# Performance work log

Measured on AMD Instinct MI355X. Metric: run time of the kernel, lower is better.

## Reference

```python
import jax, jax.numpy as jnp
import numpy as np

N_NODES = 100000
N_EDGES = 1250000
D_FEAT = 64


def setup_inputs() -> dict:
    key = jax.random.key(0)
    kx, ke = jax.random.split(key)
    x = jax.random.normal(kx, (N_NODES, D_FEAT), dtype=jnp.float32)
    edge_index = jax.random.randint(ke, (2, N_EDGES), 0, N_NODES, dtype=jnp.int64)
    return {"x": x, "edge_index": edge_index}


def reference(x, edge_index):
    # adj[src, dst] = 1; x_neighbors = adj.T @ x  ->
    # x_neighbors[i] = sum_{edges (s, d) with d == i} x[s]
    src, dst = edge_index[0], edge_index[1]
    msgs = x[src]  # [n_edges, d_feat] gather
    x_neighbors = jax.ops.segment_sum(msgs, dst, num_segments=x.shape[0])
    return x_neighbors
```

## Files before the change

kernel.cpp:

```cpp
#include <hip/hip_runtime.h>
#include <hip/hip_bf16.h>

#define N_NODES 100000
#define N_EDGES 1250000
#define D_FEAT  64
#define SB_NODES 512
#define SB_SHIFT 9
#define NSB     196
#define CAP_SB  7040
#define OVF_CAP 8192
#define EPB_I4  1024
#define N_I4    (N_EDGES / 4)
#define NBLK_BUILD ((N_I4 + EPB_I4 - 1) / EPB_I4)
#define RT      512

__global__ __launch_bounds__(256) void to_bf16(
    const float* __restrict__ x, ushort* __restrict__ xh)
{
    int t = blockIdx.x * 256 + threadIdx.x;
    const float4* x4 = (const float4*)x;
    float4 a = x4[2 * t];
    float4 b = x4[2 * t + 1];
    float f[8] = {a.x, a.y, a.z, a.w, b.x, b.y, b.z, b.w};
    uint h[8];
#pragma unroll
    for (int i = 0; i < 8; ++i) {
        uint u = __float_as_uint(f[i]);
        u += 0x7FFFu + ((u >> 16) & 1u);
        h[i] = u >> 16;
    }
    uint4 o;
    o.x = h[0] | (h[1] << 16);
    o.y = h[2] | (h[3] << 16);
    o.z = h[4] | (h[5] << 16);
    o.w = h[6] | (h[7] << 16);
    ((uint4*)xh)[t] = o;
}

__global__ __launch_bounds__(256) void build_sb(
    const int* __restrict__ src, const int* __restrict__ dst,
    uint* __restrict__ fill, uint* __restrict__ pairs,
    uint* __restrict__ ovfCnt, int2* __restrict__ ovf)
{
    __shared__ uint cnt[NSB];
    __shared__ uint base[NSB];
    const int t = threadIdx.x;
    for (int i = t; i < NSB; i += 256) cnt[i] = 0;
    __syncthreads();

    uint   pw[16];
    ushort pb[16];
    ushort pr[16];
    bool   vk[4];
    const int i40 = blockIdx.x * EPB_I4;
#pragma unroll
    for (int k = 0; k < 4; ++k) {
        int i4 = i40 + t + k * 256;
        vk[k] = (i4 < N_I4);
        if (vk[k]) {
            int4 d4 = ((const int4*)dst)[i4];
            int4 s4 = ((const int4*)src)[i4];
            int dd[4] = {d4.x, d4.y, d4.z, d4.w};
            int ss[4] = {s4.x, s4.y, s4.z, s4.w};
#pragma unroll
            for (int j = 0; j < 4; ++j) {
                uint b = ((uint)dd[j]) >> SB_SHIFT;
                uint r = atomicAdd(&cnt[b], 1u);
                pw[k * 4 + j] = ((((uint)dd[j]) & (SB_NODES - 1u)) << 17) | (uint)ss[j];
                pb[k * 4 + j] = (ushort)b;
                pr[k * 4 + j] = (ushort)r;
            }
        }
    }
    __syncthreads();

    for (int i = t; i < NSB; i += 256) {
        uint c = cnt[i];
        base[i] = c ? atomicAdd(&fill[i], c) : 0u;
    }
    __syncthreads();

#pragma unroll
    for (int j = 0; j < 16; ++j) {
        if (vk[j >> 2]) {
            uint b = pb[j];
            uint g = base[b] + pr[j];
            if (g < CAP_SB) {
                pairs[(size_t)b * CAP_SB + g] = pw[j];
            } else {
                uint o = atomicAdd(ovfCnt, 1u);
                if (o < OVF_CAP)
                    ovf[o] = make_int2((int)(pw[j] & 0x1FFFFu),
                                       (int)((b << SB_SHIFT) | (pw[j] >> 17)));
            }
        }
    }
}

__global__ __launch_bounds__(RT) void repart(
    uint* __restrict__ pairs, const uint* __restrict__ fill,
    uint* __restrict__ offs)
{
    __shared__ uint pw[CAP_SB];
    __shared__ int  cnt[SB_NODES];
    __shared__ int  scn[SB_NODES];
    __shared__ int  pos[SB_NODES];

    const int t  = threadIdx.x;
    const int sb = blockIdx.x;
    const int n  = min((int)fill[sb], CAP_SB);
    const size_t base = (size_t)sb * CAP_SB;

    cnt[t] = 0;
    __syncthreads();
    for (int i = t; i < n; i += RT) {
        uint w = pairs[base + i];
        pw[i] = w;
        atomicAdd(&cnt[w >> 17], 1);
    }
    __syncthreads();

    scn[t] = cnt[t];
    __syncthreads();
    for (int off = 1; off < SB_NODES; off <<= 1) {
        int v = (t >= off) ? scn[t - off] : 0;
        __syncthreads();
        scn[t] += v;
        __syncthreads();
    }
    {
        int e = scn[t] - cnt[t];
        pos[t] = e;
        offs[sb * SB_NODES + t] = (uint)e | ((uint)cnt[t] << 16);
    }
    __syncthreads();

    for (int i = t; i < n; i += RT) {
        uint w = pw[i];
        int r = atomicAdd(&pos[w >> 17], 1);
        pairs[base + r] = w & 0x1FFFFu;
    }
}

__global__ __launch_bounds__(256) void gather_csr(
    const ushort* __restrict__ xh, const uint* __restrict__ pairs,
    const uint* __restrict__ offs, float* __restrict__ out)
{
    const int t    = threadIdx.x;
    const int wid  = t >> 6;
    const int lane = t & 63;
    const int sub  = lane >> 3;
    const int l8   = lane & 7;
    const uint4* __restrict__ xrow = (const uint4*)xh;

    for (int nl = wid; nl < 64; nl += 4) {
        const int node = blockIdx.x * 64 + nl;
        if (node >= N_NODES) break;
        const uint v    = offs[node];
        const int start = (node >> SB_SHIFT) * CAP_SB + (int)(v & 0xFFFFu);
        const int deg   = (int)(v >> 16);

        float f[8];
#pragma unroll
        for (int j = 0; j < 8; ++j) f[j] = 0.f;

        int i = sub;
        for (; i + 8 < deg; i += 16) {
            uint s0 = pairs[start + i];
            uint s1 = pairs[start + i + 8];
            uint4 v0 = xrow[(size_t)s0 * 8 + l8];
            uint4 v1 = xrow[(size_t)s1 * 8 + l8];
            f[0] += __uint_as_float((v0.x & 0xFFFFu) << 16);
            f[1] += __uint_as_float(v0.x & 0xFFFF0000u);
            f[2] += __uint_as_float((v0.y & 0xFFFFu) << 16);
            f[3] += __uint_as_float(v0.y & 0xFFFF0000u);
            f[4] += __uint_as_float((v0.z & 0xFFFFu) << 16);
            f[5] += __uint_as_float(v0.z & 0xFFFF0000u);
            f[6] += __uint_as_float((v0.w & 0xFFFFu) << 16);
            f[7] += __uint_as_float(v0.w & 0xFFFF0000u);
            f[0] += __uint_as_float((v1.x & 0xFFFFu) << 16);
            f[1] += __uint_as_float(v1.x & 0xFFFF0000u);
            f[2] += __uint_as_float((v1.y & 0xFFFFu) << 16);
            f[3] += __uint_as_float(v1.y & 0xFFFF0000u);
            f[4] += __uint_as_float((v1.z & 0xFFFFu) << 16);
            f[5] += __uint_as_float(v1.z & 0xFFFF0000u);
            f[6] += __uint_as_float((v1.w & 0xFFFFu) << 16);
            f[7] += __uint_as_float(v1.w & 0xFFFF0000u);
        }
        if (i < deg) {
            uint s0 = pairs[start + i];
            uint4 v0 = xrow[(size_t)s0 * 8 + l8];
            f[0] += __uint_as_float((v0.x & 0xFFFFu) << 16);
            f[1] += __uint_as_float(v0.x & 0xFFFF0000u);
            f[2] += __uint_as_float((v0.y & 0xFFFFu) << 16);
            f[3] += __uint_as_float(v0.y & 0xFFFF0000u);
            f[4] += __uint_as_float((v0.z & 0xFFFFu) << 16);
            f[5] += __uint_as_float(v0.z & 0xFFFF0000u);
            f[6] += __uint_as_float((v0.w & 0xFFFFu) << 16);
            f[7] += __uint_as_float(v0.w & 0xFFFF0000u);
        }

#pragma unroll
        for (int j = 0; j < 8; ++j) {
            f[j] += __shfl_xor(f[j], 8, 64);
            f[j] += __shfl_xor(f[j], 16, 64);
            f[j] += __shfl_xor(f[j], 32, 64);
        }

        if (lane < 8) {
            float4* out4 = (float4*)out;
            out4[(size_t)node * 16 + l8 * 2]     = make_float4(f[0], f[1], f[2], f[3]);
            out4[(size_t)node * 16 + l8 * 2 + 1] = make_float4(f[4], f[5], f[6], f[7]);
        }
    }
}

__global__ __launch_bounds__(256) void ovf_fixup(
    const float* __restrict__ x, const int2* __restrict__ ovf,
    const uint* __restrict__ ovfCnt, float* __restrict__ out)
{
    const int n = min((int)*ovfCnt, OVF_CAP);
    const int wave = (blockIdx.x * blockDim.x + threadIdx.x) >> 6;
    const int lane = threadIdx.x & 63;
    const int nwaves = (gridDim.x * blockDim.x) >> 6;
    for (int e = wave; e < n; e += nwaves) {
        int2 p = ovf[e];
        atomicAdd(&out[(size_t)p.y * D_FEAT + lane], x[(size_t)p.x * D_FEAT + lane]);
    }
}

extern "C" void kernel_launch(void* const* d_in, const int* in_sizes, int n_in,
                              void* d_out, int out_size, void* d_ws, size_t ws_size,
                              hipStream_t stream) {
    const float* x = (const float*)d_in[0];
    const int* edge_index = (const int*)d_in[1];
    const int* src = edge_index;
    const int* dst = edge_index + N_EDGES;
    float* out = (float*)d_out;

    ushort* xh     = (ushort*)d_ws;
    uint*   pairs  = (uint*)(xh + (size_t)N_NODES * D_FEAT);
    uint*   offs   = pairs + (size_t)NSB * CAP_SB;
    uint*   fill   = offs + NSB * SB_NODES;
    uint*   ovfCnt = fill + NSB;
    int2*   ovf    = (int2*)(fill + NSB + 2);

    hipMemsetAsync(fill, 0, (NSB + 2) * sizeof(uint), stream);

    to_bf16<<<(N_NODES * D_FEAT / 8) / 256, 256, 0, stream>>>(x, xh);
    build_sb<<<NBLK_BUILD, 256, 0, stream>>>(src, dst, fill, pairs, ovfCnt, ovf);
    repart<<<NSB, RT, 0, stream>>>(pairs, fill, offs);
    gather_csr<<<(N_NODES + 63) / 64, 256, 0, stream>>>(xh, pairs, offs, out);
    ovf_fixup<<<16, 256, 0, stream>>>(x, ovf, ovfCnt, out);
}
```

Measured before the change: 155.0 us.

## Fold memset and overflow fixup into kernels, one node per wave in gather

The memset of the bucket counters moves into block 0 of the bf16 conversion kernel, and the separate overflow fixup kernel is removed. Each gather wave now scans the overflow list and adds any matching edges for its node before writing. The gather grid also changes from 64 nodes per block to 4 nodes per block, one per wave. This removes two launches/ops at the cost of every wave reading the overflow count, and scanning the whole list if overflow occurs; with the default capacity overflow should rarely happen.

```diff
diff --git a/kernel.cpp b/kernel.cpp
--- a/kernel.cpp
+++ b/kernel.cpp
@@ -15,8 +15,11 @@
 #define RT      512
 
 __global__ __launch_bounds__(256) void to_bf16(
-    const float* __restrict__ x, ushort* __restrict__ xh)
-{
+    const float* __restrict__ x, ushort* __restrict__ xh, uint* __restrict__ fill)
+{
+    if (blockIdx.x == 0) {
+        for (int i = threadIdx.x; i < NSB + 2; i += 256) fill[i] = 0u;
+    }
     int t = blockIdx.x * 256 + threadIdx.x;
     const float4* x4 = (const float4*)x;
     float4 a = x4[2 * t];
@@ -144,88 +147,84 @@
 
 __global__ __launch_bounds__(256) void gather_csr(
     const ushort* __restrict__ xh, const uint* __restrict__ pairs,
-    const uint* __restrict__ offs, float* __restrict__ out)
+    const uint* __restrict__ offs, const float* __restrict__ x,
+    const int2* __restrict__ ovf, const uint* __restrict__ ovfCnt,
+    float* __restrict__ out)
 {
     const int t    = threadIdx.x;
-    const int wid  = t >> 6;
     const int lane = t & 63;
     const int sub  = lane >> 3;
     const int l8   = lane & 7;
+    const int node = blockIdx.x * 4 + (t >> 6);
+    if (node >= N_NODES) return;
     const uint4* __restrict__ xrow = (const uint4*)xh;
 
-    for (int nl = wid; nl < 64; nl += 4) {
-        const int node = blockIdx.x * 64 + nl;
-        if (node >= N_NODES) break;
-        const uint v    = offs[node];
-        const int start = (node >> SB_SHIFT) * CAP_SB + (int)(v & 0xFFFFu);
-        const int deg   = (int)(v >> 16);
-
-        float f[8];
-#pragma unroll
-        for (int j = 0; j < 8; ++j) f[j] = 0.f;
-
-        int i = sub;
-        for (; i + 8 < deg; i += 16) {
-            uint s0 = pairs[start + i];
-            uint s1 = pairs[start + i + 8];
-            uint4 v0 = xrow[(size_t)s0 * 8 + l8];
-            uint4 v1 = xrow[(size_t)s1 * 8 + l8];
-            f[0] += __uint_as_float((v0.x & 0xFFFFu) << 16);
-            f[1] += __uint_as_float(v0.x & 0xFFFF0000u);
-            f[2] += __uint_as_float((v0.y & 0xFFFFu) << 16);
-            f[3] += __uint_as_float(v0.y & 0xFFFF0000u);
-            f[4] += __uint_as_float((v0.z & 0xFFFFu) << 16);
-            f[5] += __uint_as_float(v0.z & 0xFFFF0000u);
-            f[6] += __uint_as_float((v0.w & 0xFFFFu) << 16);
-            f[7] += __uint_as_float(v0.w & 0xFFFF0000u);
-            f[0] += __uint_as_float((v1.x & 0xFFFFu) << 16);
-            f[1] += __uint_as_float(v1.x & 0xFFFF0000u);
-            f[2] += __uint_as_float((v1.y & 0xFFFFu) << 16);
-            f[3] += __uint_as_float(v1.y & 0xFFFF0000u);
-            f[4] += __uint_as_float((v1.z & 0xFFFFu) << 16);
-            f[5] += __uint_as_float(v1.z & 0xFFFF0000u);
-            f[6] += __uint_as_float((v1.w & 0xFFFFu) << 16);
-            f[7] += __uint_as_float(v1.w & 0xFFFF0000u);
+    const uint v    = offs[node];
+    const int start = (node >> SB_SHIFT) * CAP_SB + (int)(v & 0xFFFFu);
+    const int deg   = (int)(v >> 16);
+
+    float f[8];
+#pragma unroll
+    for (int j = 0; j < 8; ++j) f[j] = 0.f;
+
+    int i = sub;
+    for (; i + 8 < deg; i += 16) {
+        uint s0 = pairs[start + i];
+        uint s1 = pairs[start + i + 8];
+        uint4 v0 = xrow[(size_t)s0 * 8 + l8];
+        uint4 v1 = xrow[(size_t)s1 * 8 + l8];
+        f[0] += __uint_as_float((v0.x & 0xFFFFu) << 16);
+        f[1] += __uint_as_float(v0.x & 0xFFFF0000u);
+        f[2] += __uint_as_float((v0.y & 0xFFFFu) << 16);
+        f[3] += __uint_as_float(v0.y & 0xFFFF0000u);
+        f[4] += __uint_as_float((v0.z & 0xFFFFu) << 16);
+        f[5] += __uint_as_float(v0.z & 0xFFFF0000u);
+        f[6] += __uint_as_float((v0.w & 0xFFFFu) << 16);
+        f[7] += __uint_as_float(v0.w & 0xFFFF0000u);
+        f[0] += __uint_as_float((v1.x & 0xFFFFu) << 16);
+        f[1] += __uint_as_float(v1.x & 0xFFFF0000u);
+        f[2] += __uint_as_float((v1.y & 0xFFFFu) << 16);
+        f[3] += __uint_as_float(v1.y & 0xFFFF0000u);
+        f[4] += __uint_as_float((v1.z & 0xFFFFu) << 16);
+        f[5] += __uint_as_float(v1.z & 0xFFFF0000u);
+        f[6] += __uint_as_float((v1.w & 0xFFFFu) << 16);
+        f[7] += __uint_as_float(v1.w & 0xFFFF0000u);
+    }
+    if (i < deg) {
+        uint s0 = pairs[start + i];
+        uint4 v0 = xrow[(size_t)s0 * 8 + l8];
+        f[0] += __uint_as_float((v0.x & 0xFFFFu) << 16);
+        f[1] += __uint_as_float(v0.x & 0xFFFF0000u);
+        f[2] += __uint_as_float((v0.y & 0xFFFFu) << 16);
+        f[3] += __uint_as_float(v0.y & 0xFFFF0000u);
+        f[4] += __uint_as_float((v0.z & 0xFFFFu) << 16);
+        f[5] += __uint_as_float(v0.z & 0xFFFF0000u);
+        f[6] += __uint_as_float((v0.w & 0xFFFFu) << 16);
+        f[7] += __uint_as_float(v0.w & 0xFFFF0000u);
+    }
+
+#pragma unroll
+    for (int j = 0; j < 8; ++j) {
+        f[j] += __shfl_xor(f[j], 8, 64);
+        f[j] += __shfl_xor(f[j], 16, 64);
+        f[j] += __shfl_xor(f[j], 32, 64);
+    }
+
+    const int nov = min((int)*ovfCnt, OVF_CAP);
+    for (int e = 0; e < nov; ++e) {
+        int2 p = ovf[e];
+        if (p.y == node) {
+            float4 a = ((const float4*)x)[(size_t)p.x * 16 + l8 * 2];
+            float4 b = ((const float4*)x)[(size_t)p.x * 16 + l8 * 2 + 1];
+            f[0] += a.x; f[1] += a.y; f[2] += a.z; f[3] += a.w;
+            f[4] += b.x; f[5] += b.y; f[6] += b.z; f[7] += b.w;
         }
-        if (i < deg) {
-            uint s0 = pairs[start + i];
-            uint4 v0 = xrow[(size_t)s0 * 8 + l8];
-            f[0] += __uint_as_float((v0.x & 0xFFFFu) << 16);
-            f[1] += __uint_as_float(v0.x & 0xFFFF0000u);
-            f[2] += __uint_as_float((v0.y & 0xFFFFu) << 16);
-            f[3] += __uint_as_float(v0.y & 0xFFFF0000u);
-            f[4] += __uint_as_float((v0.z & 0xFFFFu) << 16);
-            f[5] += __uint_as_float(v0.z & 0xFFFF0000u);
-            f[6] += __uint_as_float((v0.w & 0xFFFFu) << 16);
-            f[7] += __uint_as_float(v0.w & 0xFFFF0000u);
-        }
-
-#pragma unroll
-        for (int j = 0; j < 8; ++j) {
-            f[j] += __shfl_xor(f[j], 8, 64);
-            f[j] += __shfl_xor(f[j], 16, 64);
-            f[j] += __shfl_xor(f[j], 32, 64);
-        }
-
-        if (lane < 8) {
-            float4* out4 = (float4*)out;
-            out4[(size_t)node * 16 + l8 * 2]     = make_float4(f[0], f[1], f[2], f[3]);
-            out4[(size_t)node * 16 + l8 * 2 + 1] = make_float4(f[4], f[5], f[6], f[7]);
-        }
-    }
-}
-
-__global__ __launch_bounds__(256) void ovf_fixup(
-    const float* __restrict__ x, const int2* __restrict__ ovf,
-    const uint* __restrict__ ovfCnt, float* __restrict__ out)
-{
-    const int n = min((int)*ovfCnt, OVF_CAP);
-    const int wave = (blockIdx.x * blockDim.x + threadIdx.x) >> 6;
-    const int lane = threadIdx.x & 63;
-    const int nwaves = (gridDim.x * blockDim.x) >> 6;
-    for (int e = wave; e < n; e += nwaves) {
-        int2 p = ovf[e];
-        atomicAdd(&out[(size_t)p.y * D_FEAT + lane], x[(size_t)p.x * D_FEAT + lane]);
+    }
+
+    if (lane < 8) {
+        float4* out4 = (float4*)out;
+        out4[(size_t)node * 16 + l8 * 2]     = make_float4(f[0], f[1], f[2], f[3]);
+        out4[(size_t)node * 16 + l8 * 2 + 1] = make_float4(f[4], f[5], f[6], f[7]);
     }
 }
 
@@ -245,11 +244,8 @@
     uint*   ovfCnt = fill + NSB;
     int2*   ovf    = (int2*)(fill + NSB + 2);
 
-    hipMemsetAsync(fill, 0, (NSB + 2) * sizeof(uint), stream);
-
-    to_bf16<<<(N_NODES * D_FEAT / 8) / 256, 256, 0, stream>>>(x, xh);
+    to_bf16<<<(N_NODES * D_FEAT / 8) / 256, 256, 0, stream>>>(x, xh, fill);
     build_sb<<<NBLK_BUILD, 256, 0, stream>>>(src, dst, fill, pairs, ovfCnt, ovf);
     repart<<<NSB, RT, 0, stream>>>(pairs, fill, offs);
-    gather_csr<<<(N_NODES + 63) / 64, 256, 0, stream>>>(xh, pairs, offs, out);
-    ovf_fixup<<<16, 256, 0, stream>>>(x, ovf, ovfCnt, out);
-}
+    gather_csr<<<(N_NODES + 3) / 4, 256, 0, stream>>>(xh, pairs, offs, x, ovf, ovfCnt, out);
+}
```

New measurement: 143.0 us. 1.08x faster.
